# Optimization experiments

Measured on AMD Instinct MI355X. Metric: run time of the kernel, lower is better.

Reference implementation:

```python
import jax, jax.numpy as jnp
import numpy as np

B, N_I, N_H1, N_H2, N_H3, N_H4 = 4096, 1024, 1024, 1024, 2048, 1024


def _linear_params(key, n_out, n_in, gain=1.0):
    kw, kb = jax.random.split(key)
    # xavier_uniform on weight, torch default uniform bias ~ U(-1/sqrt(n_in), 1/sqrt(n_in))
    limit = gain * np.sqrt(6.0 / (n_in + n_out))
    W = jax.random.uniform(kw, (n_out, n_in), jnp.float32, -limit, limit)
    bl = 1.0 / np.sqrt(n_in)
    b = jax.random.uniform(kb, (n_out,), jnp.float32, -bl, bl)
    return W, b


def setup_inputs() -> dict:
    key = jax.random.key(0)
    ks = jax.random.split(key, 16)
    inp = {
        "X": jax.random.normal(ks[0], (B, N_I), jnp.float32),
        "hidden1": jax.random.normal(ks[1], (B, N_H1), jnp.float32),
        "hidden2": jax.random.normal(ks[2], (B, N_H2), jnp.float32),
        "cell1": jax.random.normal(ks[3], (B, N_H1), jnp.float32),
        "cell2": jax.random.normal(ks[4], (B, N_H2), jnp.float32),
    }
    # LSTM1 gates: Linear(n_i + n_h1, n_h1)
    inp["Wf1"], inp["bf1"] = _linear_params(ks[5], N_H1, N_I + N_H1, 1.0)
    inp["Wi1"], inp["bi1"] = _linear_params(ks[6], N_H1, N_I + N_H1, 1.0)
    inp["Wc1"], inp["bc1"] = _linear_params(ks[7], N_H1, N_I + N_H1, 5.0 / 3.0)
    inp["Wo1"], inp["bo1"] = _linear_params(ks[8], N_H1, N_I + N_H1, 1.0)
    # LSTM2 gates: Linear(n_h1 + n_h2, n_h2)
    inp["Wf2"], inp["bf2"] = _linear_params(ks[9], N_H2, N_H1 + N_H2, 1.0)
    inp["Wi2"], inp["bi2"] = _linear_params(ks[10], N_H2, N_H1 + N_H2, 1.0)
    inp["Wc2"], inp["bc2"] = _linear_params(ks[11], N_H2, N_H1 + N_H2, 5.0 / 3.0)
    inp["Wo2"], inp["bo2"] = _linear_params(ks[12], N_H2, N_H1 + N_H2, 1.0)
    # MLP head
    inp["W3"], inp["b3"] = _linear_params(ks[13], N_H3, N_H2, np.sqrt(2.0))
    inp["W4"], inp["b4"] = _linear_params(ks[14], N_H4, N_H3, 1.0)
    return inp


def _lstm_cell(x, h, c, Wf, bf, Wi, bi, Wc, bc, Wo, bo):
    z = jnp.concatenate([x, h], axis=1)           # [B, n_i + n_h]
    f = jax.nn.sigmoid(z @ Wf.T + bf)
    i = jax.nn.sigmoid(z @ Wi.T + bi)
    cand = jnp.tanh(z @ Wc.T + bc)
    o = jax.nn.sigmoid(z @ Wo.T + bo)
    h_new = o * jnp.tanh(cand)                    # NOTE: double tanh, faithful to source
    c_new = f * c + cand * i
    return h_new, c_new


def reference(X, hidden1, hidden2, cell1, cell2,
              Wf1, bf1, Wi1, bi1, Wc1, bc1, Wo1, bo1,
              Wf2, bf2, Wi2, bi2, Wc2, bc2, Wo2, bo2,
              W3, b3, W4, b4):
    h1, c1 = _lstm_cell(X, hidden1, cell1, Wf1, bf1, Wi1, bi1, Wc1, bc1, Wo1, bo1)
    h2, c2 = _lstm_cell(h1, hidden2, cell2, Wf2, bf2, Wi2, bi2, Wc2, bc2, Wo2, bo2)
    out3 = jax.nn.relu(h2 @ W3.T + b3)
    out = out3 @ W4.T + b4
    return (out, h1, h2, c1, c2)
```

## Files before the change

### kernel.cpp

```cpp
#include <hip/hip_runtime.h>
#include <hip/hip_bf16.h>
#include <stdint.h>

typedef unsigned short u16;
typedef __bf16 bf16x8 __attribute__((ext_vector_type(8)));
typedef float f32x4 __attribute__((ext_vector_type(4)));
typedef float f32x8 __attribute__((ext_vector_type(8)));

#define BM 128
#define BN 128
#define BK 64

struct SegArgs {
  const u16* W[4];
  const float* b[4];
  void* out[4];
  int act[4];
  int bf16out[4];
};

__device__ __forceinline__ float bf2f(u16 u) {
  union { unsigned int i; float f; } v; v.i = ((unsigned int)u) << 16; return v.f;
}
__device__ __forceinline__ u16 f2bf(float f) {
  union { float f; unsigned int i; } v; v.f = f;
  return (u16)((v.i + 0x7fffu + ((v.i >> 16) & 1u)) >> 16);
}
__device__ __forceinline__ uint4 cvt8(f32x8 v) {
  uint4 r;
  r.x = (unsigned)f2bf(v[0]) | ((unsigned)f2bf(v[1]) << 16);
  r.y = (unsigned)f2bf(v[2]) | ((unsigned)f2bf(v[3]) << 16);
  r.z = (unsigned)f2bf(v[4]) | ((unsigned)f2bf(v[5]) << 16);
  r.w = (unsigned)f2bf(v[6]) | ((unsigned)f2bf(v[7]) << 16);
  return r;
}
__device__ __forceinline__ float actf(float x, int act) {
  if (act == 1) return 1.0f / (1.0f + __expf(-x));
  if (act == 2) {
    float xc = fminf(fmaxf(x, -15.0f), 15.0f);
    float e = __expf(2.0f * xc);
    return (e - 1.0f) / (e + 1.0f);
  }
  if (act == 3) return fmaxf(x, 0.0f);
  return x;
}

struct CvtArgs { const float* src[10]; u16* dst[10]; };
__global__ void cvt_f2b(CvtArgs a) {
  const float* s = a.src[blockIdx.y];
  u16* d = a.dst[blockIdx.y];
  int i0 = (blockIdx.x * 256 + threadIdx.x) * 8;
  f32x8 v = *(const f32x8*)(s + i0);
  *(uint4*)(d + i0) = cvt8(v);
}

#define G2M 256
#define G2K 32

__global__ __launch_bounds__(512, 2) void gemm_bt2(
    const u16* __restrict__ A0, const u16* __restrict__ A1, int KA0, int K,
    SegArgs segs, int tileShift, int ldOut)
{
  __shared__ u16 smem[4 * 16384];

  const int tid  = threadIdx.x;
  const int lane = tid & 63;
  const int wave = tid >> 6;
  const int wm = wave & 1, wn = wave >> 1;
  const int mBlock  = blockIdx.x * G2M;
  const int seg     = blockIdx.y >> tileShift;
  const int nTile   = blockIdx.y & ((1 << tileShift) - 1);
  const int colBase = nTile * G2M;
  const u16* Wp = segs.W[seg];
  const int NT = K / G2K;

  auto STAGE = [&](int kt) {
    int kb = kt * G2K;
    const u16* Aseg; int ka, ldA;
    if (kb < KA0) { Aseg = A0; ka = kb;       ldA = KA0; }
    else          { Aseg = A1; ka = kb - KA0; ldA = K - KA0; }
    u16* base = &smem[(kt & 3) * 16384];
#pragma unroll
    for (int it = 0; it < 2; ++it) {
      int g   = it * 512 + tid;
      int row = g >> 2;
      int c   = (g & 3) ^ ((row >> 1) & 3);
      const u16* srcA = Aseg + (size_t)(mBlock  + row) * (size_t)ldA + (ka + c * 8);
      const u16* srcB = Wp   + (size_t)(colBase + row) * (size_t)K   + (kb + c * 8);
      u16* dA = base +        (it * 512 + wave * 64) * 8;
      u16* dB = base + 8192 + (it * 512 + wave * 64) * 8;
      __builtin_amdgcn_global_load_lds((void*)srcA, (void*)dA, 16, 0, 0);
      __builtin_amdgcn_global_load_lds((void*)srcB, (void*)dB, 16, 0, 0);
    }
  };

  const f32x4 zero = {0.f, 0.f, 0.f, 0.f};
  f32x4 acc[8][4];
#pragma unroll
  for (int m = 0; m < 8; ++m)
#pragma unroll
    for (int n = 0; n < 4; ++n) acc[m][n] = zero;

  STAGE(0); STAGE(1); STAGE(2);

  for (int t = 0; t < NT; ++t) {
    if      (t + 3 <= NT) asm volatile("s_waitcnt vmcnt(8)" ::: "memory");
    else if (t + 2 <= NT) asm volatile("s_waitcnt vmcnt(4)" ::: "memory");
    else                  asm volatile("s_waitcnt vmcnt(0)" ::: "memory");
    __builtin_amdgcn_sched_barrier(0);
    __builtin_amdgcn_s_barrier();
    __builtin_amdgcn_sched_barrier(0);

    if (t + 3 < NT) STAGE(t + 3);

    const u16* Ab = &smem[(t & 3) * 16384];
    const u16* Bb = Ab + 8192;
    const int q = lane >> 4;
    bf16x8 af[8], bfr[4];
#pragma unroll
    for (int m = 0; m < 8; ++m) {
      int r = wm * 128 + m * 16 + (lane & 15);
      int p = q ^ ((r >> 1) & 3);
      af[m] = *(const bf16x8*)(Ab + (r * 4 + p) * 8);
    }
#pragma unroll
    for (int n = 0; n < 4; ++n) {
      int r = wn * 64 + n * 16 + (lane & 15);
      int p = q ^ ((r >> 1) & 3);
      bfr[n] = *(const bf16x8*)(Bb + (r * 4 + p) * 8);
    }
    __builtin_amdgcn_s_setprio(1);
#pragma unroll
    for (int m = 0; m < 8; ++m)
#pragma unroll
      for (int n = 0; n < 4; ++n)
        acc[m][n] = __builtin_amdgcn_mfma_f32_16x16x32_bf16(af[m], bfr[n], acc[m][n], 0, 0, 0);
    __builtin_amdgcn_s_setprio(0);
  }

  const float* bp = segs.b[seg];
  const int act  = segs.act[seg];
  const int isBf = segs.bf16out[seg];
  u16*   opb = (u16*)segs.out[seg];
  float* opf = (float*)segs.out[seg];
  const int q4 = (lane >> 4) * 4;
  const int cl = lane & 15;
#pragma unroll
  for (int n = 0; n < 4; ++n) {
    int col = colBase + wn * 64 + n * 16 + cl;
    float bv = bp[col];
#pragma unroll
    for (int m = 0; m < 8; ++m) {
      int row = mBlock + wm * 128 + m * 16 + q4;
#pragma unroll
      for (int r = 0; r < 4; ++r) {
        float v = actf(acc[m][n][r] + bv, act);
        size_t idx = (size_t)(row + r) * (size_t)ldOut + col;
        if (isBf) opb[idx] = f2bf(v); else opf[idx] = v;
      }
    }
  }
}

__global__ __launch_bounds__(256, 2) void gemm_bt(
    const u16* __restrict__ A0, const u16* __restrict__ A1, int KA0, int K,
    SegArgs segs, int tileShift, int ldOut)
{
  __shared__ u16 As[BM * BK];
  __shared__ u16 Bs[BN * BK];

  const int tid  = threadIdx.x;
  const int lane = tid & 63;
  const int wave = tid >> 6;
  const int mBlock = blockIdx.x * BM;
  const int seg   = blockIdx.y >> tileShift;
  const int nTile = blockIdx.y & ((1 << tileShift) - 1);

  const u16* Wp = segs.W[seg];
  const int wm = wave & 1, wn = wave >> 1;

  const f32x4 zero = {0.f, 0.f, 0.f, 0.f};
  f32x4 acc[4][4];
#pragma unroll
  for (int i = 0; i < 4; ++i)
#pragma unroll
    for (int j = 0; j < 4; ++j) acc[i][j] = zero;

  for (int kb = 0; kb < K; kb += BK) {
    const u16* Aseg; int ka; int ldA;
    if (kb < KA0) { Aseg = A0; ka = kb;       ldA = KA0; }
    else          { Aseg = A1; ka = kb - KA0; ldA = K - KA0; }

#pragma unroll
    for (int it = 0; it < 4; ++it) {
      int s = it * 256 + tid;
      int m = s >> 3;
      int p = s & 7;
      int kc = p ^ (m & 7);
      const u16* srcA = Aseg + (size_t)(mBlock + m) * (size_t)ldA + (ka + kc * 8);
      const u16* srcB = Wp + (size_t)(nTile * BN + m) * (size_t)K + (kb + kc * 8);
      u16* dA = &As[(it * 256 + wave * 64) * 8];
      u16* dB = &Bs[(it * 256 + wave * 64) * 8];
      __builtin_amdgcn_global_load_lds((void*)srcA, (void*)dA, 16, 0, 0);
      __builtin_amdgcn_global_load_lds((void*)srcB, (void*)dB, 16, 0, 0);
    }
    __syncthreads();

#pragma unroll
    for (int ko = 0; ko < 2; ++ko) {
      bf16x8 af[4], bfr[4];
      int kcb = ko * 4 + (lane >> 4);
      int p = kcb ^ (lane & 7);
#pragma unroll
      for (int t = 0; t < 4; ++t) {
        int ml = wm * 64 + t * 16 + (lane & 15);
        af[t]  = *(const bf16x8*)&As[(ml * 8 + p) * 8];
        int nl = wn * 64 + t * 16 + (lane & 15);
        bfr[t] = *(const bf16x8*)&Bs[(nl * 8 + p) * 8];
      }
#pragma unroll
      for (int tm = 0; tm < 4; ++tm)
#pragma unroll
        for (int tn = 0; tn < 4; ++tn)
          acc[tm][tn] = __builtin_amdgcn_mfma_f32_16x16x32_bf16(af[tm], bfr[tn], acc[tm][tn], 0, 0, 0);
    }
    __syncthreads();
  }

  const float* bp = segs.b[seg];
  const int act = segs.act[seg];
  const int isBf = segs.bf16out[seg];
  u16*   opb = (u16*)segs.out[seg];
  float* opf = (float*)segs.out[seg];
  const int q  = lane >> 4;
  const int cl = lane & 15;
#pragma unroll
  for (int tn = 0; tn < 4; ++tn) {
    int col = nTile * BN + wn * 64 + tn * 16 + cl;
    float bv = bp[col];
#pragma unroll
    for (int tm = 0; tm < 4; ++tm) {
      int row = mBlock + wm * 64 + tm * 16 + q * 4;
#pragma unroll
      for (int r = 0; r < 4; ++r) {
        float v = actf(acc[tm][tn][r] + bv, act);
        size_t idx = (size_t)(row + r) * (size_t)ldOut + col;
        if (isBf) opb[idx] = f2bf(v); else opf[idx] = v;
      }
    }
  }
}

__global__ void lstm_ew(const u16* __restrict__ gates, const float* __restrict__ cold,
                        float* __restrict__ hout, float* __restrict__ cout,
                        u16* __restrict__ hb, int n)
{
  int i0 = (blockIdx.x * blockDim.x + threadIdx.x) * 8;
  if (i0 >= n) return;
  union U { uint4 v; u16 u[8]; };
  U F, I, C, O;
  F.v = *(const uint4*)(gates + i0);
  I.v = *(const uint4*)(gates + (size_t)n + i0);
  C.v = *(const uint4*)(gates + 2 * (size_t)n + i0);
  O.v = *(const uint4*)(gates + 3 * (size_t)n + i0);
  f32x8 c0v = *(const f32x8*)(cold + i0);
  f32x8 H, CN;
#pragma unroll
  for (int j = 0; j < 8; ++j) {
    float f  = bf2f(F.u[j]);
    float ig = bf2f(I.u[j]);
    float cd = bf2f(C.u[j]);
    float o  = bf2f(O.u[j]);
    float cn = f * c0v[j] + cd * ig;
    float e  = __expf(2.0f * cd);
    float th = (e - 1.0f) / (e + 1.0f);
    H[j]  = o * th;
    CN[j] = cn;
  }
  *(f32x8*)(hout + i0) = H;
  *(f32x8*)(cout + i0) = CN;
  *(uint4*)(hb + i0) = cvt8(H);
}

extern "C" void kernel_launch(void* const* d_in, const int* in_sizes, int n_in,
                              void* d_out, int out_size, void* d_ws, size_t ws_size,
                              hipStream_t stream)
{
  const size_t P   = 4096ull * 1024ull;
  const size_t C2M = 2097152ull;

  const float* X   = (const float*)d_in[0];
  const float* h1i = (const float*)d_in[1];
  const float* h2i = (const float*)d_in[2];
  const float* c1i = (const float*)d_in[3];
  const float* c2i = (const float*)d_in[4];
  const float* Wf1 = (const float*)d_in[5];  const float* bf1_ = (const float*)d_in[6];
  const float* Wi1 = (const float*)d_in[7];  const float* bi1_ = (const float*)d_in[8];
  const float* Wc1 = (const float*)d_in[9];  const float* bc1_ = (const float*)d_in[10];
  const float* Wo1 = (const float*)d_in[11]; const float* bo1_ = (const float*)d_in[12];
  const float* Wf2 = (const float*)d_in[13]; const float* bf2_ = (const float*)d_in[14];
  const float* Wi2 = (const float*)d_in[15]; const float* bi2_ = (const float*)d_in[16];
  const float* Wc2 = (const float*)d_in[17]; const float* bc2_ = (const float*)d_in[18];
  const float* Wo2 = (const float*)d_in[19]; const float* bo2_ = (const float*)d_in[20];
  const float* W3  = (const float*)d_in[21]; const float* b3_  = (const float*)d_in[22];
  const float* W4  = (const float*)d_in[23]; const float* b4_  = (const float*)d_in[24];

  float* out = (float*)d_out;
  float* h1  = out + P;
  float* h2  = out + 2 * P;
  float* c1  = out + 3 * P;
  float* c2  = out + 4 * P;

  char* ws = (char*)d_ws;
  u16* gates = (u16*)ws;
  u16* Areg  = (u16*)(ws + (32ull << 20));
  u16* Breg  = (u16*)(ws + (48ull << 20));
  u16* Creg  = (u16*)(ws + (56ull << 20));
  u16* Ereg  = (u16*)(ws + (64ull << 20));
  u16* Freg  = (u16*)(ws + (72ull << 20));

  dim3 blk(256, 1, 1);
  dim3 blk2(512, 1, 1);

  CvtArgs ca;
  ca.src[0]=Wf1;        ca.dst[0]=Areg;
  ca.src[1]=Wi1;        ca.dst[1]=Areg + C2M;
  ca.src[2]=Wc1;        ca.dst[2]=Areg + 2*C2M;
  ca.src[3]=Wo1;        ca.dst[3]=Areg + 3*C2M;
  ca.src[4]=X;          ca.dst[4]=Breg;
  ca.src[5]=X + C2M;    ca.dst[5]=Breg + C2M;
  ca.src[6]=h1i;        ca.dst[6]=Creg;
  ca.src[7]=h1i + C2M;  ca.dst[7]=Creg + C2M;
  ca.src[8]=W3;         ca.dst[8]=Freg;
  ca.src[9]=W4;         ca.dst[9]=Freg + C2M;
  cvt_f2b<<<dim3(1024, 10, 1), blk, 0, stream>>>(ca);

  SegArgs s1;
  s1.W[0]=Areg; s1.W[1]=Areg+C2M; s1.W[2]=Areg+2*C2M; s1.W[3]=Areg+3*C2M;
  s1.b[0]=bf1_; s1.b[1]=bi1_; s1.b[2]=bc1_; s1.b[3]=bo1_;
  s1.out[0]=gates; s1.out[1]=gates+P; s1.out[2]=gates+2*P; s1.out[3]=gates+3*P;
  s1.act[0]=1; s1.act[1]=1; s1.act[2]=2; s1.act[3]=1;
  s1.bf16out[0]=s1.bf16out[1]=s1.bf16out[2]=s1.bf16out[3]=1;
  gemm_bt2<<<dim3(16,16,1), blk2, 0, stream>>>(Breg, Creg, 1024, 2048, s1, 2, 1024);
  lstm_ew<<<dim3(2048,1,1), blk, 0, stream>>>(gates, c1i, h1, c1, Ereg, (int)P);

  CvtArgs cb;
  cb.src[0]=Wf2;        cb.dst[0]=Areg;
  cb.src[1]=Wi2;        cb.dst[1]=Areg + C2M;
  cb.src[2]=Wc2;        cb.dst[2]=Areg + 2*C2M;
  cb.src[3]=Wo2;        cb.dst[3]=Areg + 3*C2M;
  cb.src[4]=h2i;        cb.dst[4]=Breg;
  cb.src[5]=h2i + C2M;  cb.dst[5]=Breg + C2M;
  cvt_f2b<<<dim3(1024, 6, 1), blk, 0, stream>>>(cb);

  SegArgs s2 = s1;
  s2.b[0]=bf2_; s2.b[1]=bi2_; s2.b[2]=bc2_; s2.b[3]=bo2_;
  gemm_bt2<<<dim3(16,16,1), blk2, 0, stream>>>(Ereg, Breg, 1024, 2048, s2, 2, 1024);
  lstm_ew<<<dim3(2048,1,1), blk, 0, stream>>>(gates, c2i, h2, c2, Creg, (int)P);

  SegArgs s3;
  for (int g = 0; g < 4; ++g) { s3.W[g]=Freg; s3.b[g]=b3_; s3.out[g]=Areg; s3.act[g]=3; s3.bf16out[g]=1; }
  gemm_bt<<<dim3(32,16,1), blk, 0, stream>>>(Creg, (const u16*)nullptr, 1024, 1024, s3, 4, 2048);

  SegArgs s4;
  for (int g = 0; g < 4; ++g) { s4.W[g]=Freg+C2M; s4.b[g]=b4_; s4.out[g]=out; s4.act[g]=0; s4.bf16out[g]=0; }
  gemm_bt<<<dim3(32,8,1), blk, 0, stream>>>(Areg, (const u16*)nullptr, 2048, 2048, s4, 3, 1024);
}
```

Before: 499.4 us.

## Rewrite LSTM gate GEMM as 8-phase ping-pong pipeline with BK=64 tiles

Replaces the 4-stage BK=32 gate GEMM with a double-buffered BK=64 kernel. Each k-tile is split into four phases that interleave LDS fragment reads, quarter-tile global-to-LDS prefetches and MFMA quads, with barriers between phases. The aim is to overlap global loads and LDS reads with MFMA work at a finer grain, using a new 8-wide XOR swizzle. It adds many more barriers per tile, which could cost more than the overlap gains.

```diff
diff --git a/kernel.cpp b/kernel.cpp
--- a/kernel.cpp
+++ b/kernel.cpp
@@ -54,43 +54,116 @@
   *(uint4*)(d + i0) = cvt8(v);
 }
 
-#define G2M 256
-#define G2K 32
-
-__global__ __launch_bounds__(512, 2) void gemm_bt2(
+
+#define FENCE  asm volatile("" ::: "memory")
+#define SCHED0 __builtin_amdgcn_sched_barrier(0)
+
+#define PH_SYNC do { \
+  FENCE; SCHED0; \
+  __builtin_amdgcn_s_barrier(); \
+  asm volatile("s_waitcnt lgkmcnt(0)" ::: "memory"); \
+  SCHED0; \
+} while (0)
+
+#define PH_SYNC_VM(NOTLAST) do { \
+  FENCE; SCHED0; \
+  if (NOTLAST) asm volatile("s_waitcnt vmcnt(6)" ::: "memory"); \
+  else         asm volatile("s_waitcnt vmcnt(0)" ::: "memory"); \
+  __builtin_amdgcn_s_barrier(); \
+  asm volatile("s_waitcnt lgkmcnt(0)" ::: "memory"); \
+  SCHED0; \
+} while (0)
+
+#define PH_END do { \
+  SCHED0; FENCE; \
+  __builtin_amdgcn_s_barrier(); \
+  SCHED0; \
+} while (0)
+
+#define QUAD(MQ) do { \
+  __builtin_amdgcn_s_setprio(1); \
+  _Pragma("unroll") for (int kk = 0; kk < 2; ++kk) \
+  _Pragma("unroll") for (int mi = 0; mi < 2; ++mi) \
+  _Pragma("unroll") for (int n = 0; n < 4; ++n) \
+    acc[(MQ) * 2 + mi][n] = __builtin_amdgcn_mfma_f32_16x16x32_bf16( \
+        a2[mi][kk], bfr[n][kk], acc[(MQ) * 2 + mi][n], 0, 0, 0); \
+  __builtin_amdgcn_s_setprio(0); \
+} while (0)
+
+__global__ __launch_bounds__(512, 2) void gemm8p(
     const u16* __restrict__ A0, const u16* __restrict__ A1, int KA0, int K,
     SegArgs segs, int tileShift, int ldOut)
 {
-  __shared__ u16 smem[4 * 16384];
+  __shared__ u16 smem[2 * 32768];
 
   const int tid  = threadIdx.x;
   const int lane = tid & 63;
   const int wave = tid >> 6;
   const int wm = wave & 1, wn = wave >> 1;
-  const int mBlock  = blockIdx.x * G2M;
+  const int mBlock  = blockIdx.x * 256;
   const int seg     = blockIdx.y >> tileShift;
   const int nTile   = blockIdx.y & ((1 << tileShift) - 1);
-  const int colBase = nTile * G2M;
+  const int colBase = nTile * 256;
   const u16* Wp = segs.W[seg];
-  const int NT = K / G2K;
-
-  auto STAGE = [&](int kt) {
-    int kb = kt * G2K;
-    const u16* Aseg; int ka, ldA;
-    if (kb < KA0) { Aseg = A0; ka = kb;       ldA = KA0; }
-    else          { Aseg = A1; ka = kb - KA0; ldA = K - KA0; }
-    u16* base = &smem[(kt & 3) * 16384];
-#pragma unroll
-    for (int it = 0; it < 2; ++it) {
-      int g   = it * 512 + tid;
-      int row = g >> 2;
-      int c   = (g & 3) ^ ((row >> 1) & 3);
-      const u16* srcA = Aseg + (size_t)(mBlock  + row) * (size_t)ldA + (ka + c * 8);
-      const u16* srcB = Wp   + (size_t)(colBase + row) * (size_t)K   + (kb + c * 8);
-      u16* dA = base +        (it * 512 + wave * 64) * 8;
-      u16* dB = base + 8192 + (it * 512 + wave * 64) * 8;
-      __builtin_amdgcn_global_load_lds((void*)srcA, (void*)dA, 16, 0, 0);
-      __builtin_amdgcn_global_load_lds((void*)srcB, (void*)dB, 16, 0, 0);
+  const int NT  = K >> 6;
+  const int NIT = NT >> 1;
+
+  const int rowoff = tid >> 3;
+  const int csw    = (tid & 7) ^ (rowoff & 7);
+
+  auto STAGE = [&](int kt, int which) {
+    if (kt >= NT) return;
+    const int kb = kt << 6;
+    u16* base = &smem[(kt & 1) * 32768];
+    if (which < 2) {
+      const int r0 = which << 7;
+#pragma unroll
+      for (int h = 0; h < 2; ++h) {
+        const int rb = r0 + (h << 6);
+        const u16* src = Wp + (size_t)(colBase + rb + rowoff) * (size_t)K + (kb + csw * 8);
+        u16* dst = base + 16384 + rb * 64 + wave * 512;
+        __builtin_amdgcn_global_load_lds((void*)src, (void*)dst, 16, 0, 0);
+      }
+    } else {
+      const u16* Aseg; int ka, ldA;
+      if (kb < KA0) { Aseg = A0; ka = kb;       ldA = KA0; }
+      else          { Aseg = A1; ka = kb - KA0; ldA = K - KA0; }
+      const int r0 = (which & 1) << 6;
+#pragma unroll
+      for (int h = 0; h < 2; ++h) {
+        const int rb = r0 + (h << 7);
+        const u16* src = Aseg + (size_t)(mBlock + rb + rowoff) * (size_t)ldA + (ka + csw * 8);
+        u16* dst = base + rb * 64 + wave * 512;
+        __builtin_amdgcn_global_load_lds((void*)src, (void*)dst, 16, 0, 0);
+      }
+    }
+  };
+
+  const int rl = lane & 15;
+  const int qk = lane >> 4;
+
+  auto LDA = [&](bf16x8 (&a2)[2][2], int bufb, int mq) {
+#pragma unroll
+    for (int mi = 0; mi < 2; ++mi) {
+      const int r = wm * 128 + ((mq * 2 + mi) << 4) + rl;
+      const int rowb = bufb + r * 64;
+#pragma unroll
+      for (int kk = 0; kk < 2; ++kk) {
+        const int s = (qk + kk * 4) ^ (r & 7);
+        a2[mi][kk] = *(const bf16x8*)&smem[rowb + s * 8];
+      }
+    }
+  };
+  auto LDBf = [&](bf16x8 (&b)[4][2], int bufb) {
+#pragma unroll
+    for (int n = 0; n < 4; ++n) {
+      const int r = wn * 64 + (n << 4) + rl;
+      const int rowb = bufb + 16384 + r * 64;
+#pragma unroll
+      for (int kk = 0; kk < 2; ++kk) {
+        const int s = (qk + kk * 4) ^ (r & 7);
+        b[n][kk] = *(const bf16x8*)&smem[rowb + s * 8];
+      }
     }
   };
 
@@ -101,41 +174,35 @@
 #pragma unroll
     for (int n = 0; n < 4; ++n) acc[m][n] = zero;
 
-  STAGE(0); STAGE(1); STAGE(2);
-
-  for (int t = 0; t < NT; ++t) {
-    if      (t + 3 <= NT) asm volatile("s_waitcnt vmcnt(8)" ::: "memory");
-    else if (t + 2 <= NT) asm volatile("s_waitcnt vmcnt(4)" ::: "memory");
-    else                  asm volatile("s_waitcnt vmcnt(0)" ::: "memory");
-    __builtin_amdgcn_sched_barrier(0);
-    __builtin_amdgcn_s_barrier();
-    __builtin_amdgcn_sched_barrier(0);
-
-    if (t + 3 < NT) STAGE(t + 3);
-
-    const u16* Ab = &smem[(t & 3) * 16384];
-    const u16* Bb = Ab + 8192;
-    const int q = lane >> 4;
-    bf16x8 af[8], bfr[4];
-#pragma unroll
-    for (int m = 0; m < 8; ++m) {
-      int r = wm * 128 + m * 16 + (lane & 15);
-      int p = q ^ ((r >> 1) & 3);
-      af[m] = *(const bf16x8*)(Ab + (r * 4 + p) * 8);
-    }
-#pragma unroll
-    for (int n = 0; n < 4; ++n) {
-      int r = wn * 64 + n * 16 + (lane & 15);
-      int p = q ^ ((r >> 1) & 3);
-      bfr[n] = *(const bf16x8*)(Bb + (r * 4 + p) * 8);
-    }
-    __builtin_amdgcn_s_setprio(1);
-#pragma unroll
-    for (int m = 0; m < 8; ++m)
-#pragma unroll
-      for (int n = 0; n < 4; ++n)
-        acc[m][n] = __builtin_amdgcn_mfma_f32_16x16x32_bf16(af[m], bfr[n], acc[m][n], 0, 0, 0);
-    __builtin_amdgcn_s_setprio(0);
+  STAGE(0, 0); STAGE(0, 1); STAGE(0, 2); STAGE(0, 3);
+  STAGE(1, 0); STAGE(1, 1); STAGE(1, 2);
+  asm volatile("s_waitcnt vmcnt(6)" ::: "memory");
+  SCHED0;
+  __builtin_amdgcn_s_barrier();
+  SCHED0;
+
+  for (int i = 0; i < NIT; ++i) {
+    const int t0 = 2 * i;
+    const bool notLast = (i + 1 < NIT);
+    bf16x8 a2[2][2], bfr[4][2];
+
+    LDBf(bfr, 0); LDA(a2, 0, 0); STAGE(t0 + 1, 3);
+    PH_SYNC; QUAD(0); PH_END;
+    LDA(a2, 0, 1); STAGE(t0 + 2, 0);
+    PH_SYNC; QUAD(1); PH_END;
+    LDA(a2, 0, 2); STAGE(t0 + 2, 1);
+    PH_SYNC; QUAD(2); PH_END;
+    LDA(a2, 0, 3); STAGE(t0 + 2, 2);
+    PH_SYNC_VM(notLast); QUAD(3); PH_END;
+
+    LDBf(bfr, 32768); LDA(a2, 32768, 0); STAGE(t0 + 2, 3);
+    PH_SYNC; QUAD(0); PH_END;
+    LDA(a2, 32768, 1); STAGE(t0 + 3, 0);
+    PH_SYNC; QUAD(1); PH_END;
+    LDA(a2, 32768, 2); STAGE(t0 + 3, 1);
+    PH_SYNC; QUAD(2); PH_END;
+    LDA(a2, 32768, 3); STAGE(t0 + 3, 2);
+    PH_SYNC_VM(notLast); QUAD(3); PH_END;
   }
 
   const float* bp = segs.b[seg];
@@ -341,7 +408,7 @@
   s1.out[0]=gates; s1.out[1]=gates+P; s1.out[2]=gates+2*P; s1.out[3]=gates+3*P;
   s1.act[0]=1; s1.act[1]=1; s1.act[2]=2; s1.act[3]=1;
   s1.bf16out[0]=s1.bf16out[1]=s1.bf16out[2]=s1.bf16out[3]=1;
-  gemm_bt2<<<dim3(16,16,1), blk2, 0, stream>>>(Breg, Creg, 1024, 2048, s1, 2, 1024);
+  gemm8p<<<dim3(16,16,1), blk2, 0, stream>>>(Breg, Creg, 1024, 2048, s1, 2, 1024);
   lstm_ew<<<dim3(2048,1,1), blk, 0, stream>>>(gates, c1i, h1, c1, Ereg, (int)P);
 
   CvtArgs cb;
@@ -355,7 +422,7 @@
 
   SegArgs s2 = s1;
   s2.b[0]=bf2_; s2.b[1]=bi2_; s2.b[2]=bc2_; s2.b[3]=bo2_;
-  gemm_bt2<<<dim3(16,16,1), blk2, 0, stream>>>(Ereg, Breg, 1024, 2048, s2, 2, 1024);
+  gemm8p<<<dim3(16,16,1), blk2, 0, stream>>>(Ereg, Breg, 1024, 2048, s2, 2, 1024);
   lstm_ew<<<dim3(2048,1,1), blk, 0, stream>>>(gates, c2i, h2, c2, Creg, (int)P);
 
   SegArgs s3;
```

New measurement: 497.4 us. About the same (-0.4%).
